# Kernel tuning notes

Hardware: AMD Instinct MI355X
Metric: run time of the kernel (lower is better)

The kernel has to match this reference:

```python
import jax, jax.numpy as jnp
import numpy as np

B, N, D = 16, 96, 128
NUM_TOKENS, NUM_CLASSES = 14, 10
NUM_ROUNDS = 5


def setup_inputs() -> dict:
    key = jax.random.key(0)
    ks = jax.random.split(key, 8)
    def lin(k, fan_in, shape):
        return (jax.random.normal(k, shape, jnp.float32) / np.sqrt(fan_in)).astype(jnp.float32)
    return {
        "tok": jax.random.randint(ks[0], (B, N), 0, NUM_TOKENS),
        "A": jax.random.uniform(ks[1], (B, N, N), jnp.float32),
        "embed_W": jax.random.normal(ks[2], (NUM_TOKENS, D), jnp.float32),
        "W1": lin(ks[3], 2 * D, (2 * D, D)),   # msg_fc1, stored [in, out]
        "b1": jnp.zeros((D,), jnp.float32),
        "W2": lin(ks[4], D, (D, D)),           # msg_fc2
        "b2": jnp.zeros((D,), jnp.float32),
        "Wo1": lin(ks[5], D, (D, D)),          # out_fc1
        "bo1": jnp.zeros((D,), jnp.float32),
        "Wo2": lin(ks[6], D, (D, NUM_CLASSES)),  # out_fc2 (no bias)
        "alpha": 0, "tau": 1, "beta": 0, "hard": 0,
    }


def reference(tok, A, embed_W, W1, b1, W2, b2, Wo1, bo1, Wo2, alpha, tau, beta, hard):
    # tok: [B,N] int, A: [B,N,N]. Dropout in eval mode (identity).
    e = embed_W[tok]                      # [B,N,D] token embeddings
    centroids = embed_W[4:]               # [10,D]
    W1e, W1x = W1[:D], W1[D:]             # split of msg_fc1 over the concat [e_i ; x_j]
    e_proj = jnp.einsum('bid,de->bie', e, W1e)  # constant across rounds

    def head(x2d):  # out_fc2(relu(out_fc1(x)))
        return jnp.maximum(x2d @ Wo1 + bo1, 0.0) @ Wo2

    def discretize(x):
        logits = head(x.reshape(-1, D))
        # beta=0, hard=False: gumbel_softmax degenerates to tempered softmax
        a = jax.nn.softmax(logits / tau, axis=-1)
        return (a @ centroids).reshape(x.shape)

    x = e
    for r in range(NUM_ROUNDS):
        xj_proj = jnp.einsum('bjd,de->bje', x, W1x)
        # h[b,i,j] = relu(msg_fc1([e_i ; x_j])) without materializing the concat
        h = jnp.maximum(e_proj[:, :, None, :] + xj_proj[:, None, :, :] + b1, 0.0)  # [B,N,N,D]
        m = jnp.maximum(jnp.einsum('bijd,de->bije', h, W2) + b2, 0.0)
        agg = jnp.einsum('bji,bijd->bid', A, m)  # A^T masked sum over j
        x = x + agg
        if r < NUM_ROUNDS - 1:
            # resid=True, alpha=0 -> np.random.random() > 0 a.s. -> residual add
            x = x + discretize(x)
    out = head(x[:, 0, :])                                  # [B,10]
    x_all = head(x.reshape(-1, D)).reshape(B, N, NUM_CLASSES)  # [B,N,10]
    return out, x_all
```

## Files before the change

kernel.cpp:

```cpp
#include <hip/hip_runtime.h>
#include <hip/hip_bf16.h>
#include <math.h>

#define BB   16
#define NN   96
#define DD   128
#define NCLS 10

typedef __attribute__((ext_vector_type(8))) short bf16x8;
typedef __attribute__((ext_vector_type(8))) unsigned short u16x8;
typedef __attribute__((ext_vector_type(4))) float f32x4;

__device__ __forceinline__ float scalar_as_float(int v) {
    if (v >= -1000000 && v <= 1000000) return (float)v;
    return __int_as_float(v);
}
__device__ __forceinline__ unsigned short f2bf(float f) {
    unsigned u = __float_as_uint(f);
    return (unsigned short)((u + 0x7FFFu + ((u >> 16) & 1u)) >> 16);
}
__device__ __forceinline__ float bf2f(unsigned short h) {
    return __uint_as_float(((unsigned)h) << 16);
}

#define MFMA(A, B, C) __builtin_amdgcn_mfma_f32_16x16x32_bf16(A, B, C, 0, 0, 0)

__global__ __launch_bounds__(256) void k_prep(
    const int* __restrict__ tok, const float* __restrict__ A,
    const float* __restrict__ embed_W, const float* __restrict__ W1,
    const float* __restrict__ W2, const float* __restrict__ Wo1,
    float* __restrict__ x, float* __restrict__ e_proj,
    unsigned short* __restrict__ xjA, float* __restrict__ AT,
    unsigned short* __restrict__ w2hi, unsigned short* __restrict__ w1xb,
    unsigned short* __restrict__ wo1b)
{
    const int bx = blockIdx.x;
    const int t  = threadIdx.x;
    const float* W1x = W1 + DD * DD;

    if (bx < 384) {
        __shared__ float e_s[4][DD];
        const int rbase = bx * 4;
        const int rh = t >> 7, h = t & 127;
        const int r0 = rh * 2, r1 = rh * 2 + 1;
        {
            const float e0 = embed_W[tok[rbase + r0] * DD + h];
            const float e1 = embed_W[tok[rbase + r1] * DD + h];
            e_s[r0][h] = e0;  x[(rbase + r0) * DD + h] = e0;
            e_s[r1][h] = e1;  x[(rbase + r1) * DD + h] = e1;
        }
        __syncthreads();
        float a10 = 0.f, a11 = 0.f, a20 = 0.f, a21 = 0.f;
#pragma unroll 8
        for (int k = 0; k < DD; ++k) {
            const float w1v  = W1[k * DD + h];
            const float w1xv = W1x[k * DD + h];
            a10 = fmaf(e_s[r0][k], w1v,  a10);
            a11 = fmaf(e_s[r1][k], w1v,  a11);
            a20 = fmaf(e_s[r0][k], w1xv, a20);
            a21 = fmaf(e_s[r1][k], w1xv, a21);
        }
        e_proj[(rbase + r0) * DD + h] = a10;
        e_proj[(rbase + r1) * DD + h] = a11;
        xjA[(rbase + r0) * DD + h] = f2bf(a20);
        xjA[(rbase + r1) * DD + h] = f2bf(a21);
    } else if (bx < 400) {
        const int b = bx - 384;
        __shared__ float tile[NN][NN + 1];
        for (int idx = t; idx < NN * NN; idx += 256)
            tile[idx / NN][idx % NN] = A[b * NN * NN + idx];
        __syncthreads();
        for (int idx = t; idx < NN * NN; idx += 256) {
            const int i = idx / NN, j = idx % NN;
            AT[b * NN * NN + idx] = tile[j][i];
        }
    } else if (bx < 408) {
        const int dt = bx - 400;
        const int kc = t >> 6, ll = t & 63;
        const int base = ((dt * 4 + kc) * 64 + ll) * 8;
        const int c = dt * 16 + (ll & 15);
#pragma unroll
        for (int e = 0; e < 8; ++e)
            w2hi[base + e] = f2bf(W2[(kc * 32 + (ll >> 4) * 8 + e) * DD + c]);
    } else if (bx < 412) {
        const int base = (bx - 408) * 4096 + t * 16;
#pragma unroll
        for (int e = 0; e < 16; ++e) w1xb[base + e] = f2bf(W1x[base + e]);
    } else {
        const int base = (bx - 412) * 4096 + t * 16;
#pragma unroll
        for (int e = 0; e < 16; ++e) wo1b[base + e] = f2bf(Wo1[base + e]);
    }
}

template<int FIN>
__global__ __launch_bounds__(512, 4) void k_round(
    const float* __restrict__ AT, const float* __restrict__ e_proj,
    const unsigned short* __restrict__ xj_in, const float* __restrict__ b1,
    const unsigned short* __restrict__ w2hi, const float* __restrict__ b2,
    const float* __restrict__ Wo1, const unsigned short* __restrict__ wo1b,
    const float* __restrict__ bo1, const float* __restrict__ Wo2,
    const float* __restrict__ embed_W, const unsigned short* __restrict__ w1xb,
    const int* __restrict__ tau_p,
    float* __restrict__ x, unsigned short* __restrict__ xj_out,
    float* __restrict__ out, float* __restrict__ x_all)
{
    const int bx = blockIdx.x;
    const int b  = bx >> 5;
    const int is = bx & 31;
    const int t  = threadIdx.x;
    const int w  = t >> 6;
    const int l  = t & 63;
    const int jg  = w >> 2;
    const int dg  = w & 3;
    const int jg3 = jg * 3;
    const int d0 = (t & 15) * 8;
    const int row0 = b * NN + is;

    __shared__ __align__(16) unsigned short hs[2][NN * DD];
    __shared__ float ac_s[2][NN];
    __shared__ float agg_part[3][2][DD];
    __shared__ float xn_s[3][DD];
    __shared__ float part_s[4][3][DD];

    const bf16x8* WH = (const bf16x8*)w2hi;
    const int f0 = (dg * 4) * 64 + l;
    const int f1 = ((dg + 4) * 4) * 64 + l;
    bf16x8 bh00 = WH[f0],        bh10 = WH[f1];
    bf16x8 bh01 = WH[f0 + 64],   bh11 = WH[f1 + 64];
    bf16x8 bh02 = WH[f0 + 128],  bh12 = WH[f1 + 128];
    bf16x8 bh03 = WH[f0 + 192],  bh13 = WH[f1 + 192];
    asm volatile("" : "+v"(bh00), "+v"(bh01), "+v"(bh02), "+v"(bh03),
                      "+v"(bh10), "+v"(bh11), "+v"(bh12), "+v"(bh13));
    const float b2v0 = b2[dg * 16 + (l & 15)];
    const float b2v1 = b2[64 + dg * 16 + (l & 15)];
    const float4 b4a = *(const float4*)(b1 + d0);
    const float4 b4b = *(const float4*)(b1 + d0 + 4);
    const u16x8* xj8 = (const u16x8*)(xj_in + b * NN * DD);

    auto STAGE = [&](int u, int p) {
        const int row_u = row0 + 32 * u;
        const float4 ea = *(const float4*)(e_proj + row_u * DD + d0);
        const float4 eb = *(const float4*)(e_proj + row_u * DD + d0 + 4);
        float v8[8];
        v8[0] = ea.x + b4a.x; v8[1] = ea.y + b4a.y;
        v8[2] = ea.z + b4a.z; v8[3] = ea.w + b4a.w;
        v8[4] = eb.x + b4b.x; v8[5] = eb.y + b4b.y;
        v8[6] = eb.z + b4b.z; v8[7] = eb.w + b4b.w;
        if (t < NN) ac_s[p][t] = AT[row_u * NN + t];
#pragma unroll
        for (int it = 0; it < 3; ++it) {
            const int idx8 = t + it * 512;
            const int j = idx8 >> 4;
            const u16x8 xv = xj8[idx8];
            u16x8 hh;
#pragma unroll
            for (int e = 0; e < 8; ++e)
                hh[e] = f2bf(fmaxf(bf2f(xv[e]) + v8[e], 0.f));
            *(u16x8*)&hs[p][(j * DD + d0) ^ ((j & 7) << 3)] = hh;
        }
    };

    auto GEMM = [&](int u, int p) {
        float aggp0 = 0.f, aggp1 = 0.f;
        const unsigned short* hb = hs[p];
#pragma unroll
        for (int jj = 0; jj < 3; ++jj) {
            const int jt  = jg3 + jj;
            const int r16 = jt * 16 + (l & 15);
            const int ko  = (l >> 4) * 8;
            const int sw  = (r16 & 7) << 3;
            const bf16x8 a0 = *(const bf16x8*)&hb[(r16 * DD + ko     ) ^ sw];
            const bf16x8 a1 = *(const bf16x8*)&hb[(r16 * DD + ko + 32) ^ sw];
            const bf16x8 a2 = *(const bf16x8*)&hb[(r16 * DD + ko + 64) ^ sw];
            const bf16x8 a3 = *(const bf16x8*)&hb[(r16 * DD + ko + 96) ^ sw];
            f32x4 c0 = {0.f, 0.f, 0.f, 0.f}, c1 = {0.f, 0.f, 0.f, 0.f};
            c0 = MFMA(a0, bh00, c0);  c1 = MFMA(a0, bh10, c1);
            c0 = MFMA(a1, bh01, c0);  c1 = MFMA(a1, bh11, c1);
            c0 = MFMA(a2, bh02, c0);  c1 = MFMA(a2, bh12, c1);
            c0 = MFMA(a3, bh03, c0);  c1 = MFMA(a3, bh13, c1);
#pragma unroll
            for (int r = 0; r < 4; ++r) {
                const float a = ac_s[p][jt * 16 + (l >> 4) * 4 + r];
                aggp0 = fmaf(a, fmaxf(c0[r] + b2v0, 0.f), aggp0);
                aggp1 = fmaf(a, fmaxf(c1[r] + b2v1, 0.f), aggp1);
            }
        }
        aggp0 += __shfl_xor(aggp0, 16); aggp0 += __shfl_xor(aggp0, 32);
        aggp1 += __shfl_xor(aggp1, 16); aggp1 += __shfl_xor(aggp1, 32);
        if (l < 16) {
            agg_part[u][jg][dg * 16 + l]      = aggp0;
            agg_part[u][jg][64 + dg * 16 + l] = aggp1;
        }
    };

    STAGE(0, 0);
    __syncthreads();
    STAGE(1, 1);
    GEMM(0, 0);
    __syncthreads();
    STAGE(2, 0);
    GEMM(1, 1);
    __syncthreads();
    GEMM(2, 0);
    __syncthreads();

    float xr0 = 0.f, xr1 = 0.f;
    if (w < 3) {
        const int row_u = row0 + 32 * w;
        xr0 = x[row_u * DD + l]      + agg_part[w][0][l]      + agg_part[w][1][l];
        xr1 = x[row_u * DD + l + 64] + agg_part[w][0][l + 64] + agg_part[w][1][l + 64];
        xn_s[w][l]      = xr0;
        xn_s[w][l + 64] = xr1;
    }
    __syncthreads();

    {
        const int q = t >> 7, h = t & 127;
        float p0 = 0.f, p1 = 0.f, p2 = 0.f;
#pragma unroll
        for (int kk = 0; kk < 32; ++kk) {
            const int k = q * 32 + kk;
            const float wv = FIN ? Wo1[k * DD + h] : bf2f(wo1b[k * DD + h]);
            p0 = fmaf(xn_s[0][k], wv, p0);
            p1 = fmaf(xn_s[1][k], wv, p1);
            p2 = fmaf(xn_s[2][k], wv, p2);
        }
        part_s[q][0][h] = p0; part_s[q][1][h] = p1; part_s[q][2][h] = p2;
    }
    __syncthreads();

    if (w < 3) {
        const int row_u = row0 + 32 * w;
        const float hid0 = fmaxf(part_s[0][w][l] + part_s[1][w][l]
                               + part_s[2][w][l] + part_s[3][w][l] + bo1[l], 0.f);
        const float hid1 = fmaxf(part_s[0][w][l + 64] + part_s[1][w][l + 64]
                               + part_s[2][w][l + 64] + part_s[3][w][l + 64] + bo1[l + 64], 0.f);
        float lgp[NCLS];
#pragma unroll
        for (int c = 0; c < NCLS; ++c)
            lgp[c] = hid0 * Wo2[l * NCLS + c] + hid1 * Wo2[(l + 64) * NCLS + c];
#pragma unroll
        for (int s = 1; s < 64; s <<= 1) {
#pragma unroll
            for (int c = 0; c < NCLS; ++c) lgp[c] += __shfl_xor(lgp[c], s);
        }
        if (FIN) {
#pragma unroll
            for (int c = 0; c < NCLS; ++c) {
                if (l == c) {
                    x_all[row_u * NCLS + c] = lgp[c];
                    if (is == 0 && w == 0) out[b * NCLS + c] = lgp[c];
                }
            }
        } else {
            float mx = -1e30f;
#pragma unroll
            for (int c = 0; c < NCLS; ++c) mx = fmaxf(mx, lgp[c]);
            const float inv_tau = 1.f / scalar_as_float(tau_p[0]);
            float p[NCLS], den = 0.f;
#pragma unroll
            for (int c = 0; c < NCLS; ++c) { p[c] = expf((lgp[c] - mx) * inv_tau); den += p[c]; }
            const float invden = 1.f / den;
#pragma unroll
            for (int c = 0; c < NCLS; ++c) {
                const float pc = p[c] * invden;
                xr0 = fmaf(pc, embed_W[(4 + c) * DD + l], xr0);
                xr1 = fmaf(pc, embed_W[(4 + c) * DD + l + 64], xr1);
            }
            x[row_u * DD + l]      = xr0;
            x[row_u * DD + l + 64] = xr1;
            xn_s[w][l]      = xr0;
            xn_s[w][l + 64] = xr1;
        }
    }
    if (FIN) return;
    __syncthreads();

    {
        const int q = t >> 7, h = t & 127;
        float p0 = 0.f, p1 = 0.f, p2 = 0.f;
#pragma unroll
        for (int kk = 0; kk < 32; ++kk) {
            const int k = q * 32 + kk;
            const float wv = bf2f(w1xb[k * DD + h]);
            p0 = fmaf(xn_s[0][k], wv, p0);
            p1 = fmaf(xn_s[1][k], wv, p1);
            p2 = fmaf(xn_s[2][k], wv, p2);
        }
        part_s[q][0][h] = p0; part_s[q][1][h] = p1; part_s[q][2][h] = p2;
    }
    __syncthreads();

    if (w < 3) {
        const int row_u = row0 + 32 * w;
        xj_out[row_u * DD + l] =
            f2bf(part_s[0][w][l] + part_s[1][w][l] + part_s[2][w][l] + part_s[3][w][l]);
        xj_out[row_u * DD + l + 64] =
            f2bf(part_s[0][w][l + 64] + part_s[1][w][l + 64]
               + part_s[2][w][l + 64] + part_s[3][w][l + 64]);
    }
}

extern "C" void kernel_launch(void* const* d_in, const int* in_sizes, int n_in,
                              void* d_out, int out_size, void* d_ws, size_t ws_size,
                              hipStream_t stream)
{
    (void)in_sizes; (void)n_in; (void)out_size; (void)ws_size;
    const int*   tok     = (const int*)d_in[0];
    const float* Aab     = (const float*)d_in[1];
    const float* embed_W = (const float*)d_in[2];
    const float* W1      = (const float*)d_in[3];
    const float* b1      = (const float*)d_in[4];
    const float* W2      = (const float*)d_in[5];
    const float* b2      = (const float*)d_in[6];
    const float* Wo1     = (const float*)d_in[7];
    const float* bo1     = (const float*)d_in[8];
    const float* Wo2     = (const float*)d_in[9];
    const int*   tau_p   = (const int*)d_in[11];

    float* out   = (float*)d_out;
    float* x_all = out + BB * NCLS;

    float* ws     = (float*)d_ws;
    float* x      = ws;
    float* e_proj = ws + BB * NN * DD;
    float* ATr    = ws + 2 * BB * NN * DD;
    unsigned short* xjA  = (unsigned short*)(ws + 2 * BB * NN * DD + BB * NN * NN);
    unsigned short* xjB  = xjA + BB * NN * DD;
    unsigned short* w2hi = xjB + BB * NN * DD;
    unsigned short* w1xb = w2hi + DD * DD;
    unsigned short* wo1b = w1xb + DD * DD;

    k_prep<<<416, 256, 0, stream>>>(tok, Aab, embed_W, W1, W2, Wo1,
                                    x, e_proj, xjA, ATr, w2hi, w1xb, wo1b);
    for (int r = 0; r < 5; ++r) {
        const unsigned short* xin = (r & 1) ? xjB : xjA;
        unsigned short*       xot = (r & 1) ? xjA : xjB;
        if (r < 4)
            k_round<0><<<512, 512, 0, stream>>>(ATr, e_proj, xin, b1, w2hi, b2,
                                                Wo1, wo1b, bo1, Wo2, embed_W, w1xb,
                                                tau_p, x, xot, out, x_all);
        else
            k_round<1><<<512, 512, 0, stream>>>(ATr, e_proj, xin, b1, w2hi, b2,
                                                Wo1, wo1b, bo1, Wo2, embed_W, w1xb,
                                                tau_p, x, xot, out, x_all);
    }
}
```

Before: 84.67 us.

## Replace first message-passing round with token-pair message table lookup

Because x equals the token embeddings in round 0, the message MLP output depends only on the (token_i, token_j) pair. A 14x14xD table is precomputed in the prep kernel, and a lightweight round-0 kernel aggregates A-weighted table rows, skipping the N×N×D MFMA GEMM for that round. The per-row e_proj projection is also replaced by a per-token table with b1 folded in. This adds a small serial table-building cost to the prep kernel and slightly changes bf16 rounding order.

```diff
diff --git a/kernel.cpp b/kernel.cpp
--- a/kernel.cpp
+++ b/kernel.cpp
@@ -6,6 +6,7 @@
 #define NN   96
 #define DD   128
 #define NCLS 10
+#define NTOK 14
 
 typedef __attribute__((ext_vector_type(8))) short bf16x8;
 typedef __attribute__((ext_vector_type(8))) unsigned short u16x8;
@@ -26,11 +27,11 @@
 #define MFMA(A, B, C) __builtin_amdgcn_mfma_f32_16x16x32_bf16(A, B, C, 0, 0, 0)
 
 __global__ __launch_bounds__(256) void k_prep(
-    const int* __restrict__ tok, const float* __restrict__ A,
-    const float* __restrict__ embed_W, const float* __restrict__ W1,
-    const float* __restrict__ W2, const float* __restrict__ Wo1,
-    float* __restrict__ x, float* __restrict__ e_proj,
-    unsigned short* __restrict__ xjA, float* __restrict__ AT,
+    const float* __restrict__ A, const float* __restrict__ embed_W,
+    const float* __restrict__ W1, const float* __restrict__ b1,
+    const float* __restrict__ W2, const float* __restrict__ b2,
+    const float* __restrict__ Wo1,
+    float* __restrict__ Mtab, float* __restrict__ t2tab, float* __restrict__ AT,
     unsigned short* __restrict__ w2hi, unsigned short* __restrict__ w1xb,
     unsigned short* __restrict__ wo1b)
 {
@@ -38,34 +39,41 @@
     const int t  = threadIdx.x;
     const float* W1x = W1 + DD * DD;
 
-    if (bx < 384) {
-        __shared__ float e_s[4][DD];
-        const int rbase = bx * 4;
-        const int rh = t >> 7, h = t & 127;
-        const int r0 = rh * 2, r1 = rh * 2 + 1;
+    if (bx < NTOK * NTOK) {
+        const int ti = bx / NTOK, tj = bx % NTOK;
+        const int d = t & 127, half = t >> 7;
+        __shared__ float part[2][DD];
+        __shared__ unsigned short hb[DD];
         {
-            const float e0 = embed_W[tok[rbase + r0] * DD + h];
-            const float e1 = embed_W[tok[rbase + r1] * DD + h];
-            e_s[r0][h] = e0;  x[(rbase + r0) * DD + h] = e0;
-            e_s[r1][h] = e1;  x[(rbase + r1) * DD + h] = e1;
+            const float* erow  = embed_W + (half ? tj : ti) * DD;
+            const float* wbase = half ? W1x : W1;
+            float acc = 0.f;
+#pragma unroll 8
+            for (int k = 0; k < DD; ++k)
+                acc = fmaf(erow[k], wbase[k * DD + d], acc);
+            part[half][d] = acc;
         }
         __syncthreads();
-        float a10 = 0.f, a11 = 0.f, a20 = 0.f, a21 = 0.f;
+        if (half == 0) {
+            const float v = part[0][d] + b1[d];
+            if (tj == 0) t2tab[ti * DD + d] = v;
+            hb[d] = f2bf(fmaxf(v + part[1][d], 0.f));
+        }
+        __syncthreads();
+        {
+            float m = 0.f;
 #pragma unroll 8
-        for (int k = 0; k < DD; ++k) {
-            const float w1v  = W1[k * DD + h];
-            const float w1xv = W1x[k * DD + h];
-            a10 = fmaf(e_s[r0][k], w1v,  a10);
-            a11 = fmaf(e_s[r1][k], w1v,  a11);
-            a20 = fmaf(e_s[r0][k], w1xv, a20);
-            a21 = fmaf(e_s[r1][k], w1xv, a21);
-        }
-        e_proj[(rbase + r0) * DD + h] = a10;
-        e_proj[(rbase + r1) * DD + h] = a11;
-        xjA[(rbase + r0) * DD + h] = f2bf(a20);
-        xjA[(rbase + r1) * DD + h] = f2bf(a21);
-    } else if (bx < 400) {
-        const int b = bx - 384;
+            for (int kk = 0; kk < 64; ++kk) {
+                const int k = half * 64 + kk;
+                m = fmaf(bf2f(hb[k]), bf2f(f2bf(W2[k * DD + d])), m);
+            }
+            part[half][d] = m;
+        }
+        __syncthreads();
+        if (half == 0)
+            Mtab[(ti * NTOK + tj) * DD + d] = fmaxf(part[0][d] + part[1][d] + b2[d], 0.f);
+    } else if (bx < 212) {
+        const int b = bx - 196;
         __shared__ float tile[NN][NN + 1];
         for (int idx = t; idx < NN * NN; idx += 256)
             tile[idx / NN][idx % NN] = A[b * NN * NN + idx];
@@ -74,29 +82,168 @@
             const int i = idx / NN, j = idx % NN;
             AT[b * NN * NN + idx] = tile[j][i];
         }
-    } else if (bx < 408) {
-        const int dt = bx - 400;
+    } else if (bx < 220) {
+        const int dt = bx - 212;
         const int kc = t >> 6, ll = t & 63;
         const int base = ((dt * 4 + kc) * 64 + ll) * 8;
         const int c = dt * 16 + (ll & 15);
 #pragma unroll
         for (int e = 0; e < 8; ++e)
             w2hi[base + e] = f2bf(W2[(kc * 32 + (ll >> 4) * 8 + e) * DD + c]);
-    } else if (bx < 412) {
-        const int base = (bx - 408) * 4096 + t * 16;
+    } else if (bx < 224) {
+        const int base = (bx - 220) * 4096 + t * 16;
 #pragma unroll
         for (int e = 0; e < 16; ++e) w1xb[base + e] = f2bf(W1x[base + e]);
     } else {
-        const int base = (bx - 412) * 4096 + t * 16;
+        const int base = (bx - 224) * 4096 + t * 16;
 #pragma unroll
         for (int e = 0; e < 16; ++e) wo1b[base + e] = f2bf(Wo1[base + e]);
+    }
+}
+
+__global__ __launch_bounds__(512, 4) void k_round0(
+    const int* __restrict__ tok, const float* __restrict__ AT,
+    const float* __restrict__ Mtab, const float* __restrict__ embed_W,
+    const unsigned short* __restrict__ wo1b, const float* __restrict__ bo1,
+    const float* __restrict__ Wo2, const unsigned short* __restrict__ w1xb,
+    const int* __restrict__ tau_p,
+    float* __restrict__ x, unsigned short* __restrict__ xj_out)
+{
+    const int bx = blockIdx.x;
+    const int b  = bx >> 5;
+    const int is = bx & 31;
+    const int t  = threadIdx.x;
+    const int w  = t >> 6;
+    const int l  = t & 63;
+    const int row0 = b * NN + is;
+
+    __shared__ __align__(16) float mt[3][NTOK * DD];
+    __shared__ float at3[3][NN];
+    __shared__ int   tkj[NN];
+    __shared__ float agg_s[3][DD];
+    __shared__ float xn_s[3][DD];
+    __shared__ float part_s[4][3][DD];
+
+    const int ti0 = tok[row0], ti1 = tok[row0 + 32], ti2 = tok[row0 + 64];
+    if (t < NN) {
+        tkj[t]    = tok[b * NN + t];
+        at3[0][t] = AT[row0 * NN + t];
+        at3[1][t] = AT[(row0 + 32) * NN + t];
+        at3[2][t] = AT[(row0 + 64) * NN + t];
+    }
+    for (int idx = t; idx < 3 * NTOK * DD; idx += 512) {
+        const int u = idx / (NTOK * DD), rd = idx - u * (NTOK * DD);
+        const int tiu = (u == 0) ? ti0 : ((u == 1) ? ti1 : ti2);
+        mt[u][rd] = Mtab[tiu * NTOK * DD + rd];
+    }
+    __syncthreads();
+
+    if (t < 192) {
+        const int u = t >> 6, d2 = t & 63;
+        const float2* mtu = (const float2*)mt[u];
+        float2 acc = {0.f, 0.f};
+#pragma unroll 4
+        for (int j = 0; j < NN; ++j) {
+            const float a = at3[u][j];
+            const float2 m = mtu[tkj[j] * 64 + d2];
+            acc.x = fmaf(a, m.x, acc.x);
+            acc.y = fmaf(a, m.y, acc.y);
+        }
+        *(float2*)&agg_s[u][d2 * 2] = acc;
+    }
+    __syncthreads();
+
+    float xr0 = 0.f, xr1 = 0.f;
+    if (w < 3) {
+        const int tk = (w == 0) ? ti0 : ((w == 1) ? ti1 : ti2);
+        xr0 = embed_W[tk * DD + l]      + agg_s[w][l];
+        xr1 = embed_W[tk * DD + l + 64] + agg_s[w][l + 64];
+        xn_s[w][l]      = xr0;
+        xn_s[w][l + 64] = xr1;
+    }
+    __syncthreads();
+
+    {
+        const int q = t >> 7, h = t & 127;
+        float p0 = 0.f, p1 = 0.f, p2 = 0.f;
+#pragma unroll
+        for (int kk = 0; kk < 32; ++kk) {
+            const int k = q * 32 + kk;
+            const float wv = bf2f(wo1b[k * DD + h]);
+            p0 = fmaf(xn_s[0][k], wv, p0);
+            p1 = fmaf(xn_s[1][k], wv, p1);
+            p2 = fmaf(xn_s[2][k], wv, p2);
+        }
+        part_s[q][0][h] = p0; part_s[q][1][h] = p1; part_s[q][2][h] = p2;
+    }
+    __syncthreads();
+
+    if (w < 3) {
+        const int row_u = row0 + 32 * w;
+        const float hid0 = fmaxf(part_s[0][w][l] + part_s[1][w][l]
+                               + part_s[2][w][l] + part_s[3][w][l] + bo1[l], 0.f);
+        const float hid1 = fmaxf(part_s[0][w][l + 64] + part_s[1][w][l + 64]
+                               + part_s[2][w][l + 64] + part_s[3][w][l + 64] + bo1[l + 64], 0.f);
+        float lgp[NCLS];
+#pragma unroll
+        for (int c = 0; c < NCLS; ++c)
+            lgp[c] = hid0 * Wo2[l * NCLS + c] + hid1 * Wo2[(l + 64) * NCLS + c];
+#pragma unroll
+        for (int s = 1; s < 64; s <<= 1) {
+#pragma unroll
+            for (int c = 0; c < NCLS; ++c) lgp[c] += __shfl_xor(lgp[c], s);
+        }
+        float mx = -1e30f;
+#pragma unroll
+        for (int c = 0; c < NCLS; ++c) mx = fmaxf(mx, lgp[c]);
+        const float inv_tau = 1.f / scalar_as_float(tau_p[0]);
+        float p[NCLS], den = 0.f;
+#pragma unroll
+        for (int c = 0; c < NCLS; ++c) { p[c] = expf((lgp[c] - mx) * inv_tau); den += p[c]; }
+        const float invden = 1.f / den;
+#pragma unroll
+        for (int c = 0; c < NCLS; ++c) {
+            const float pc = p[c] * invden;
+            xr0 = fmaf(pc, embed_W[(4 + c) * DD + l], xr0);
+            xr1 = fmaf(pc, embed_W[(4 + c) * DD + l + 64], xr1);
+        }
+        x[row_u * DD + l]      = xr0;
+        x[row_u * DD + l + 64] = xr1;
+        xn_s[w][l]      = xr0;
+        xn_s[w][l + 64] = xr1;
+    }
+    __syncthreads();
+
+    {
+        const int q = t >> 7, h = t & 127;
+        float p0 = 0.f, p1 = 0.f, p2 = 0.f;
+#pragma unroll
+        for (int kk = 0; kk < 32; ++kk) {
+            const int k = q * 32 + kk;
+            const float wv = bf2f(w1xb[k * DD + h]);
+            p0 = fmaf(xn_s[0][k], wv, p0);
+            p1 = fmaf(xn_s[1][k], wv, p1);
+            p2 = fmaf(xn_s[2][k], wv, p2);
+        }
+        part_s[q][0][h] = p0; part_s[q][1][h] = p1; part_s[q][2][h] = p2;
+    }
+    __syncthreads();
+
+    if (w < 3) {
+        const int row_u = row0 + 32 * w;
+        xj_out[row_u * DD + l] =
+            f2bf(part_s[0][w][l] + part_s[1][w][l] + part_s[2][w][l] + part_s[3][w][l]);
+        xj_out[row_u * DD + l + 64] =
+            f2bf(part_s[0][w][l + 64] + part_s[1][w][l + 64]
+               + part_s[2][w][l + 64] + part_s[3][w][l + 64]);
     }
 }
 
 template<int FIN>
 __global__ __launch_bounds__(512, 4) void k_round(
-    const float* __restrict__ AT, const float* __restrict__ e_proj,
-    const unsigned short* __restrict__ xj_in, const float* __restrict__ b1,
+    const int* __restrict__ tok, const float* __restrict__ AT,
+    const float* __restrict__ t2tab,
+    const unsigned short* __restrict__ xj_in,
     const unsigned short* __restrict__ w2hi, const float* __restrict__ b2,
     const float* __restrict__ Wo1, const unsigned short* __restrict__ wo1b,
     const float* __restrict__ bo1, const float* __restrict__ Wo2,
@@ -123,6 +270,8 @@
     __shared__ float xn_s[3][DD];
     __shared__ float part_s[4][3][DD];
 
+    const int tk0 = tok[row0], tk1 = tok[row0 + 32], tk2 = tok[row0 + 64];
+
     const bf16x8* WH = (const bf16x8*)w2hi;
     const int f0 = (dg * 4) * 64 + l;
     const int f1 = ((dg + 4) * 4) * 64 + l;
@@ -134,19 +283,16 @@
                       "+v"(bh10), "+v"(bh11), "+v"(bh12), "+v"(bh13));
     const float b2v0 = b2[dg * 16 + (l & 15)];
     const float b2v1 = b2[64 + dg * 16 + (l & 15)];
-    const float4 b4a = *(const float4*)(b1 + d0);
-    const float4 b4b = *(const float4*)(b1 + d0 + 4);
     const u16x8* xj8 = (const u16x8*)(xj_in + b * NN * DD);
 
     auto STAGE = [&](int u, int p) {
         const int row_u = row0 + 32 * u;
-        const float4 ea = *(const float4*)(e_proj + row_u * DD + d0);
-        const float4 eb = *(const float4*)(e_proj + row_u * DD + d0 + 4);
+        const int tk = (u == 0) ? tk0 : ((u == 1) ? tk1 : tk2);
+        const float4 ea = *(const float4*)(t2tab + tk * DD + d0);
+        const float4 eb = *(const float4*)(t2tab + tk * DD + d0 + 4);
         float v8[8];
-        v8[0] = ea.x + b4a.x; v8[1] = ea.y + b4a.y;
-        v8[2] = ea.z + b4a.z; v8[3] = ea.w + b4a.w;
-        v8[4] = eb.x + b4b.x; v8[5] = eb.y + b4b.y;
-        v8[6] = eb.z + b4b.z; v8[7] = eb.w + b4b.w;
+        v8[0] = ea.x; v8[1] = ea.y; v8[2] = ea.z; v8[3] = ea.w;
+        v8[4] = eb.x; v8[5] = eb.y; v8[6] = eb.z; v8[7] = eb.w;
         if (t < NN) ac_s[p][t] = AT[row_u * NN + t];
 #pragma unroll
         for (int it = 0; it < 3; ++it) {
@@ -324,25 +470,28 @@
 
     float* ws     = (float*)d_ws;
     float* x      = ws;
-    float* e_proj = ws + BB * NN * DD;
-    float* ATr    = ws + 2 * BB * NN * DD;
-    unsigned short* xjA  = (unsigned short*)(ws + 2 * BB * NN * DD + BB * NN * NN);
+    float* ATr    = ws + BB * NN * DD;
+    float* Mtab   = ATr + BB * NN * NN;
+    float* t2tab  = Mtab + NTOK * NTOK * DD;
+    unsigned short* xjA  = (unsigned short*)(t2tab + NTOK * DD);
     unsigned short* xjB  = xjA + BB * NN * DD;
     unsigned short* w2hi = xjB + BB * NN * DD;
     unsigned short* w1xb = w2hi + DD * DD;
     unsigned short* wo1b = w1xb + DD * DD;
 
-    k_prep<<<416, 256, 0, stream>>>(tok, Aab, embed_W, W1, W2, Wo1,
-                                    x, e_proj, xjA, ATr, w2hi, w1xb, wo1b);
-    for (int r = 0; r < 5; ++r) {
-        const unsigned short* xin = (r & 1) ? xjB : xjA;
-        unsigned short*       xot = (r & 1) ? xjA : xjB;
+    k_prep<<<228, 256, 0, stream>>>(Aab, embed_W, W1, b1, W2, b2, Wo1,
+                                    Mtab, t2tab, ATr, w2hi, w1xb, wo1b);
+    k_round0<<<512, 512, 0, stream>>>(tok, ATr, Mtab, embed_W, wo1b, bo1,
+                                      Wo2, w1xb, tau_p, x, xjA);
+    for (int r = 1; r < 5; ++r) {
+        const unsigned short* xin = (r & 1) ? xjA : xjB;
+        unsigned short*       xot = (r & 1) ? xjB : xjA;
         if (r < 4)
-            k_round<0><<<512, 512, 0, stream>>>(ATr, e_proj, xin, b1, w2hi, b2,
+            k_round<0><<<512, 512, 0, stream>>>(tok, ATr, t2tab, xin, w2hi, b2,
                                                 Wo1, wo1b, bo1, Wo2, embed_W, w1xb,
                                                 tau_p, x, xot, out, x_all);
         else
-            k_round<1><<<512, 512, 0, stream>>>(ATr, e_proj, xin, b1, w2hi, b2,
+            k_round<1><<<512, 512, 0, stream>>>(tok, ATr, t2tab, xin, w2hi, b2,
                                                 Wo1, wo1b, bo1, Wo2, embed_W, w1xb,
                                                 tau_p, x, xot, out, x_all);
     }
```

New measurement: 79.03 us. 1.07x faster.
